# Kernel tuning notes

Measured on AMD Instinct MI355X. Metric: run time of the kernel, lower is better.

Reference implementation:

```python
import jax, jax.numpy as jnp
import numpy as np

N = 4096        # nodes
E = 131072      # edges (avg degree 32)
D = 128         # parser.d
H1, H2, H3 = 256, 128, 64   # parser.neurons_gnn
L = 2
THRESH = 0.6 ** L           # cosine-similarity cutoff used in attention()
SCALE = 0.05                # weight init scale


def setup_inputs() -> dict:
    key = jax.random.key(0)
    ks = jax.random.split(key, 14)
    X = jax.random.normal(ks[0], (N, D), dtype=jnp.float32)
    edge_index = jax.random.randint(ks[1], (2, E), 0, N, dtype=jnp.int64)
    W1 = jax.random.normal(ks[2], (D, H1), dtype=jnp.float32) * SCALE
    b1 = jnp.zeros((H1,), dtype=jnp.float32)
    a1w = jax.random.normal(ks[3], (2 * H1,), dtype=jnp.float32) * SCALE
    a1b = jnp.zeros((), dtype=jnp.float32)
    W2 = jax.random.normal(ks[4], (H1, H2), dtype=jnp.float32) * SCALE
    b2 = jnp.zeros((H2,), dtype=jnp.float32)
    a2w = jax.random.normal(ks[5], (2 * H2,), dtype=jnp.float32) * SCALE
    a2b = jnp.zeros((), dtype=jnp.float32)
    W3 = jax.random.normal(ks[6], (H2, H3), dtype=jnp.float32) * SCALE
    b3 = jnp.zeros((H3,), dtype=jnp.float32)
    return {"X": X, "edge_index": edge_index,
            "W1": W1, "b1": b1, "a1w": a1w, "a1b": a1b,
            "W2": W2, "b2": b2, "a2w": a2w, "a2b": a2b,
            "W3": W3, "b3": b3}


def _attention(h, src, dst, aw, ab):
    """Vectorized form of GNN.attention: edge-softmax neighbor aggregation
    plus dense cosine-thresholded all-pairs aggregation, averaged.
    attn_fc(cat(h_i, h_j)) = (h_i . aw_left) + (h_j . aw_right) + ab."""
    n, dh = h.shape
    al = h @ aw[:dh]            # [N] left half of attention projection
    ar = h @ aw[dh:]            # [N] right half
    # --- neighbor branch: a_ij = softmax-like normalized exp(leaky_relu(.)) over neighbors of i
    e = jnp.exp(jax.nn.leaky_relu(al[src] + ar[dst] + ab))   # [E]
    denom = jax.ops.segment_sum(e, src, num_segments=n)      # [N]
    a = e / denom[src]                                       # [E]
    h_a = h + jax.ops.segment_sum(a[:, None] * h[dst], src, num_segments=n)
    # --- dense branch: thresholded cosine similarity modulates attention score
    hn = h / jnp.linalg.norm(h, axis=1, keepdims=True)       # [N, dh]
    C = hn @ hn.T                                            # [N, N] cosine
    C = jnp.where(C <= THRESH, 0.0, C)
    S = al[:, None] + ar[None, :] + ab                       # [N, N] attn scores
    B = jnp.exp(C * jax.nn.leaky_relu(S))                    # [N, N]
    h1 = h + B @ h
    return 0.5 * (h_a + h1)


def reference(X, edge_index, W1, b1, a1w, a1b, W2, b2, a2w, a2b, W3, b3):
    src, dst = edge_index[0], edge_index[1]
    h = X @ W1 + b1
    h = _attention(h, src, dst, a1w, a1b)
    h = jax.nn.relu(h)
    h = h @ W2 + b2
    h = _attention(h, src, dst, a2w, a2b)
    h = jax.nn.relu(h)
    h = h @ W3 + b3
    # F.normalize(h, p=2, dim=1)
    h = h / jnp.maximum(jnp.linalg.norm(h, axis=1, keepdims=True), 1e-12)
    return h
```

## Files before the change

kernel.cpp:

```cpp
#include <hip/hip_runtime.h>
#include <math.h>
#include <type_traits>

#define NN 4096
#define NE 131072

typedef short short8 __attribute__((ext_vector_type(8)));
typedef float f32x4 __attribute__((ext_vector_type(4)));
typedef float f32x2 __attribute__((ext_vector_type(2)));
typedef unsigned short u16;

__device__ __forceinline__ float lrelu_f(float x) { return x > 0.0f ? x : 0.01f * x; }

__device__ __forceinline__ u16 f2bf(float x) {
  unsigned int u = __float_as_uint(x);
  unsigned int r = (u + 0x7FFF + ((u >> 16) & 1)) >> 16;
  return (u16)r;
}
__device__ __forceinline__ float bf2f(u16 b) { return __uint_as_float(((unsigned int)b) << 16); }

__device__ __forceinline__ void gload_lds16(const u16* g, u16* l) {
  __builtin_amdgcn_global_load_lds((const __attribute__((address_space(1))) void*)g,
                                   (__attribute__((address_space(3))) void*)l, 16, 0, 0);
}

__global__ __launch_bounds__(256) void wtrans_kernel(const float* __restrict__ W,
    u16* __restrict__ WThi, u16* __restrict__ WTlo, int K, int P) {
  __shared__ u16 th[32][33], tl[32][33];
  int bp = blockIdx.x, bk = blockIdx.y;
  int t = threadIdx.x, tx = t & 31, ty8 = t >> 5;
  #pragma unroll
  for (int r = 0; r < 4; ++r) {
    int k = bk * 32 + ty8 + r * 8;
    int p = bp * 32 + tx;
    float x = W[(size_t)k * P + p];
    u16 hi = f2bf(x);
    th[ty8 + r * 8][tx] = hi;
    tl[ty8 + r * 8][tx] = f2bf(x - bf2f(hi));
  }
  __syncthreads();
  #pragma unroll
  for (int r = 0; r < 4; ++r) {
    int p = bp * 32 + ty8 + r * 8;
    int k = bk * 32 + tx;
    WThi[(size_t)p * K + k] = th[tx][ty8 + r * 8];
    WTlo[(size_t)p * K + k] = tl[tx][ty8 + r * 8];
  }
}

template<bool RELU>
__global__ __launch_bounds__(256) void convert_io_kernel(const float* __restrict__ x,
    u16* __restrict__ ghi, u16* __restrict__ glo) {
  int idx = blockIdx.x * 256 + threadIdx.x;
  float v = x[idx];
  if (RELU) v = fmaxf(v, 0.0f);
  u16 hi = f2bf(v);
  ghi[idx] = hi;
  glo[idx] = f2bf(v - bf2f(hi));
}

template<int K, int P>
__global__ __launch_bounds__(256) void mgemm_kernel(
    const u16* __restrict__ Ahi, const u16* __restrict__ Alo,
    const u16* __restrict__ WThi, const u16* __restrict__ WTlo,
    const float* __restrict__ bias, float* __restrict__ O) {
  constexpr int KC = K / 32;
  int w = threadIdx.x >> 6, l = threadIdx.x & 63;
  int lr = l & 15, lk = l >> 4;
  int i0 = blockIdx.x * 16;
  int p0 = blockIdx.y * 64 + w * 16;
  const u16* arh = Ahi + (size_t)(i0 + lr) * K + lk * 8;
  const u16* arl = Alo + (size_t)(i0 + lr) * K + lk * 8;
  const u16* brh = WThi + (size_t)(p0 + lr) * K + lk * 8;
  const u16* brl = WTlo + (size_t)(p0 + lr) * K + lk * 8;
  f32x4 ahh = {0.f, 0.f, 0.f, 0.f};
  f32x4 ahl = {0.f, 0.f, 0.f, 0.f};
  f32x4 alh = {0.f, 0.f, 0.f, 0.f};
  #pragma unroll
  for (int c = 0; c < KC; ++c) {
    short8 Ah = *(const short8*)(arh + 32 * c);
    short8 Al = *(const short8*)(arl + 32 * c);
    short8 Bh = *(const short8*)(brh + 32 * c);
    short8 Bl = *(const short8*)(brl + 32 * c);
    ahh = __builtin_amdgcn_mfma_f32_16x16x32_bf16(Ah, Bh, ahh, 0, 0, 0);
    ahl = __builtin_amdgcn_mfma_f32_16x16x32_bf16(Ah, Bl, ahl, 0, 0, 0);
    alh = __builtin_amdgcn_mfma_f32_16x16x32_bf16(Al, Bh, alh, 0, 0, 0);
  }
  int p = p0 + lr;
  float bv = bias[p];
  #pragma unroll
  for (int q = 0; q < 4; ++q) {
    int i = i0 + 4 * lk + q;
    O[(size_t)i * P + p] = ahh[q] + ahl[q] + alh[q] + bv;
  }
}

template<int DH>
__global__ __launch_bounds__(256) void rowstats_kernel(const float* __restrict__ h,
    const float* __restrict__ aw, float* __restrict__ al, float* __restrict__ ar,
    float* __restrict__ inv) {
  constexpr int NC = DH / 64;
  int wid = threadIdx.x >> 6, lane = threadIdx.x & 63;
  int i = blockIdx.x * 4 + wid;
  float s2 = 0.f, sl = 0.f, sr = 0.f;
  #pragma unroll
  for (int c = 0; c < NC; ++c) {
    float x = h[(size_t)i * DH + c * 64 + lane];
    s2 = fmaf(x, x, s2);
    sl = fmaf(x, aw[c * 64 + lane], sl);
    sr = fmaf(x, aw[DH + c * 64 + lane], sr);
  }
  #pragma unroll
  for (int m = 32; m > 0; m >>= 1) {
    s2 += __shfl_xor(s2, m);
    sl += __shfl_xor(sl, m);
    sr += __shfl_xor(sr, m);
  }
  if (lane == 0) { al[i] = sl; ar[i] = sr; inv[i] = rsqrtf(s2); }
}

template<int DH>
__global__ void colsum_kernel(const float* __restrict__ h, float* __restrict__ cs) {
  int d = threadIdx.x;
  int r0 = blockIdx.x * (NN / 32);
  float s = 0.f;
  for (int i = 0; i < NN / 32; ++i) s += h[(size_t)(r0 + i) * DH + d];
  atomicAdd(&cs[d], s);
}

template<int DH>
__global__ __launch_bounds__(256) void convtrans_kernel(const float* __restrict__ h,
    u16* __restrict__ hhi, u16* __restrict__ hlo, u16* __restrict__ hT) {
  __shared__ u16 tile[32][33];
  int bx = blockIdx.x;
  int by = blockIdx.y;
  int t = threadIdx.x, tx = t & 31, ty8 = t >> 5;
  #pragma unroll
  for (int r = 0; r < 4; ++r) {
    int i = by * 32 + ty8 + r * 8;
    int d = bx * 32 + tx;
    float x = h[(size_t)i * DH + d];
    u16 hi = f2bf(x);
    hhi[(size_t)i * DH + d] = hi;
    hlo[(size_t)i * DH + d] = f2bf(x - bf2f(hi));
    tile[ty8 + r * 8][tx] = hi;
  }
  __syncthreads();
  #pragma unroll
  for (int r = 0; r < 4; ++r) {
    int d = bx * 32 + ty8 + r * 8;
    int i = by * 32 + tx;
    hT[(size_t)d * NN + i] = tile[tx][ty8 + r * 8];
  }
}

__global__ void hist_kernel(const int* __restrict__ src, int* __restrict__ counts) {
  int e = blockIdx.x * 256 + threadIdx.x;
  atomicAdd(&counts[src[e]], 1);
}

__global__ __launch_bounds__(1024) void scan_kernel(const int* __restrict__ counts,
    int* __restrict__ offsets, int* __restrict__ cursor) {
  __shared__ int part[1024];
  int t = threadIdx.x;
  int v[4]; int run = 0;
  #pragma unroll
  for (int j = 0; j < 4; ++j) { v[j] = counts[4 * t + j]; run += v[j]; }
  part[t] = run;
  __syncthreads();
  for (int off = 1; off < 1024; off <<= 1) {
    int y = (t >= off) ? part[t - off] : 0;
    __syncthreads();
    part[t] += y;
    __syncthreads();
  }
  int base = part[t] - run;
  #pragma unroll
  for (int j = 0; j < 4; ++j) { offsets[4 * t + j] = base; cursor[4 * t + j] = base; base += v[j]; }
  if (t == 1023) offsets[NN] = base;
}

__global__ void scatter_idx_kernel(const int* __restrict__ src, const int* __restrict__ dst,
    int* __restrict__ cursor, int* __restrict__ dstS) {
  int e = blockIdx.x * 256 + threadIdx.x;
  int s = src[e];
  int p = atomicAdd(&cursor[s], 1);
  dstS[p] = dst[e];
}

template<int DH>
__global__ __launch_bounds__(256) void gather_kernel(const float* __restrict__ h,
    const int* __restrict__ offsets, const int* __restrict__ dstS,
    const float* __restrict__ al, const float* __restrict__ ar,
    const float* __restrict__ ab, float* __restrict__ o) {
  constexpr int VW = DH / 64;
  using V = typename std::conditional<VW == 4, f32x4, f32x2>::type;
  int wid = threadIdx.x >> 6, lane = threadIdx.x & 63;
  int i = blockIdx.x * 4 + wid;
  int beg = offsets[i], end = offsets[i + 1];
  float base = al[i] + ab[0];
  V acc0{}, acc1{};
  float esum0 = 0.f, esum1 = 0.f;
  int k = beg;
  for (; k + 2 <= end; k += 2) {
    int d0 = dstS[k], d1 = dstS[k + 1];
    float e0 = expf(lrelu_f(base + ar[d0]));
    float e1 = expf(lrelu_f(base + ar[d1]));
    V v0 = *(const V*)&h[(size_t)d0 * DH + lane * VW];
    V v1 = *(const V*)&h[(size_t)d1 * DH + lane * VW];
    esum0 += e0; esum1 += e1;
    acc0 += e0 * v0;
    acc1 += e1 * v1;
  }
  if (k < end) {
    int d0 = dstS[k];
    float e0 = expf(lrelu_f(base + ar[d0]));
    V v0 = *(const V*)&h[(size_t)d0 * DH + lane * VW];
    esum0 += e0;
    acc0 += e0 * v0;
  }
  float esum = esum0 + esum1;
  float rd = (beg < end) ? 0.5f / esum : 0.0f;
  *(V*)&o[(size_t)i * DH + lane * VW] = (acc0 + acc1) * rd;
}

template<int DH>
__global__ __launch_bounds__(256) void qk_kernel(
    const u16* __restrict__ hhi, const u16* __restrict__ hlo,
    const float* __restrict__ al, const float* __restrict__ ar,
    const float* __restrict__ inv, const float* __restrict__ ab,
    u16* __restrict__ W, int* __restrict__ flags) {
  constexpr int KC = DH / 32;
  __shared__ u16 sA[2][2][128][32];
  __shared__ u16 sB[2][2][128][32];
  int i0 = blockIdx.x * 128;
  int j0 = blockIdx.y * 128;
  int w = threadIdx.x >> 6, l = threadIdx.x & 63;
  int wr = w >> 1, wc = w & 1;
  int lr = l & 15, lk = l >> 4;

  int rl = l >> 2;
  int sc = ((l & 3) ^ ((l >> 3) & 3)) * 8;
  const u16* gAh0 = hhi + (size_t)(i0 + 32 * w + rl) * DH + sc;
  const u16* gAl0 = hlo + (size_t)(i0 + 32 * w + rl) * DH + sc;
  const u16* gBh0 = hhi + (size_t)(j0 + 32 * w + rl) * DH + sc;
  const u16* gBl0 = hlo + (size_t)(j0 + 32 * w + rl) * DH + sc;

  f32x4 acc[4][4];
  #pragma unroll
  for (int q = 0; q < 4; ++q)
    #pragma unroll
    for (int s = 0; s < 4; ++s) acc[q][s] = (f32x4){0.f, 0.f, 0.f, 0.f};

#define QK_STAGE(buf, c) do { \
    gload_lds16(gAh0 + (c) * 32,           &sA[buf][0][32 * w][0]); \
    gload_lds16(gAh0 + 16 * DH + (c) * 32, &sA[buf][0][32 * w + 16][0]); \
    gload_lds16(gAl0 + (c) * 32,           &sA[buf][1][32 * w][0]); \
    gload_lds16(gAl0 + 16 * DH + (c) * 32, &sA[buf][1][32 * w + 16][0]); \
    gload_lds16(gBh0 + (c) * 32,           &sB[buf][0][32 * w][0]); \
    gload_lds16(gBh0 + 16 * DH + (c) * 32, &sB[buf][0][32 * w + 16][0]); \
    gload_lds16(gBl0 + (c) * 32,           &sB[buf][1][32 * w][0]); \
    gload_lds16(gBl0 + 16 * DH + (c) * 32, &sB[buf][1][32 * w + 16][0]); \
  } while (0)

  QK_STAGE(0, 0);
  __syncthreads();

  int cs = (lk ^ ((lr >> 1) & 3)) * 8;
  int cur = 0;
  for (int c = 0; c < KC; ++c) {
    if (c + 1 < KC) QK_STAGE(cur ^ 1, c + 1);
    short8 Ah[4], Al[4], Bh[4], Bl[4];
    #pragma unroll
    for (int q = 0; q < 4; ++q) {
      Ah[q] = *(const short8*)&sA[cur][0][64 * wr + 16 * q + lr][cs];
      Al[q] = *(const short8*)&sA[cur][1][64 * wr + 16 * q + lr][cs];
    }
    #pragma unroll
    for (int s = 0; s < 4; ++s) {
      Bh[s] = *(const short8*)&sB[cur][0][64 * wc + 16 * s + lr][cs];
      Bl[s] = *(const short8*)&sB[cur][1][64 * wc + 16 * s + lr][cs];
    }
    #pragma unroll
    for (int q = 0; q < 4; ++q)
      #pragma unroll
      for (int s = 0; s < 4; ++s) {
        acc[q][s] = __builtin_amdgcn_mfma_f32_16x16x32_bf16(Al[q], Bh[s], acc[q][s], 0, 0, 0);
        acc[q][s] = __builtin_amdgcn_mfma_f32_16x16x32_bf16(Ah[q], Bl[s], acc[q][s], 0, 0, 0);
        acc[q][s] = __builtin_amdgcn_mfma_f32_16x16x32_bf16(Ah[q], Bh[s], acc[q][s], 0, 0, 0);
      }
    __syncthreads();
    cur ^= 1;
  }
#undef QK_STAGE

  float abv = ab[0];
  int i_base = i0 + 64 * wr + 4 * lk;
  int j_base = j0 + 64 * wc + lr;
  float arj[4], invj[4];
  #pragma unroll
  for (int s = 0; s < 4; ++s) {
    int j = j_base + 16 * s;
    arj[s] = ar[j] + abv;
    invj[s] = inv[j];
  }
  int wany = 0;
  #pragma unroll
  for (int q = 0; q < 4; ++q) {
    float ali_[4], invi_[4];
    #pragma unroll
    for (int qq = 0; qq < 4; ++qq) {
      int i = i_base + 16 * q + qq;
      ali_[qq] = al[i];
      invi_[qq] = inv[i];
    }
    #pragma unroll
    for (int s = 0; s < 4; ++s)
      #pragma unroll
      for (int qq = 0; qq < 4; ++qq) {
        float C = acc[q][s][qq] * invi_[qq] * invj[s];
        float wv = 0.0f;
        if (C > 0.36f) wv = expm1f(C * lrelu_f(ali_[qq] + arj[s]));
        if (wv != 0.0f) wany = 1;
        W[(size_t)(i_base + 16 * q + qq) * NN + j_base + 16 * s] = f2bf(wv);
      }
  }
  int anyv = __any(wany) ? 1 : 0;
  if (l == 0)
    flags[((i0 >> 6) + wr) * 64 + (j0 >> 6) + wc] = anyv;
}

template<int DH>
__global__ __launch_bounds__(256) void pv_kernel(
    const u16* __restrict__ W, const u16* __restrict__ hT,
    const int* __restrict__ flags, const float* __restrict__ h,
    const float* __restrict__ cs, float* __restrict__ o) {
  __shared__ u16 sW[2][16][64];
  __shared__ u16 sT[2][4][16][64];
  __shared__ int list[64];
  __shared__ int nact_s;
  int ib = blockIdx.x;
  int w = threadIdx.x >> 6, l = threadIdx.x & 63;
  int lr = l & 15, lk = l >> 4;
  int i0 = ib * 16;
  int d0 = blockIdx.y * 64 + w * 16;
  const int* frow = flags + (i0 >> 6) * 64;
  if (threadIdx.x < 64) {
    int f = frow[threadIdx.x] != 0;
    unsigned long long m = __ballot(f);
    int pos = __popcll(m & ((1ULL << threadIdx.x) - 1ULL));
    if (f) list[pos] = threadIdx.x;
    if (threadIdx.x == 0) nact_s = __popcll(m);
  }
  __syncthreads();
  int nact = nact_s;

  int srow0 = l >> 3;
  int scol = ((l & 7) * 8) ^ ((srow0 & 7) << 3);
  const u16* gW0 = W + (size_t)(i0 + srow0) * NN + scol;
  const u16* gT0 = hT + (size_t)(d0 + srow0) * NN + scol;
  f32x4 acc0 = {0.f, 0.f, 0.f, 0.f};
  f32x4 acc1 = {0.f, 0.f, 0.f, 0.f};

  if (nact > 0) {
    {
      int j0 = list[0] * 64;
      if (w == 0) {
        gload_lds16(gW0 + j0, &sW[0][0][0]);
        gload_lds16(gW0 + 8 * NN + j0, &sW[0][8][0]);
      }
      gload_lds16(gT0 + j0, &sT[0][w][0][0]);
      gload_lds16(gT0 + 8 * NN + j0, &sT[0][w][8][0]);
    }
    __syncthreads();
    int cur = 0;
    for (int t = 0; t < nact; ++t) {
      if (t + 1 < nact) {
        int jn = list[t + 1] * 64;
        int nb = cur ^ 1;
        if (w == 0) {
          gload_lds16(gW0 + jn, &sW[nb][0][0]);
          gload_lds16(gW0 + 8 * NN + jn, &sW[nb][8][0]);
        }
        gload_lds16(gT0 + jn, &sT[nb][w][0][0]);
        gload_lds16(gT0 + 8 * NN + jn, &sT[nb][w][8][0]);
      }
      int sx = (lr & 7) << 3;
      short8 a0 = *(const short8*)&sW[cur][lr][(lk * 8) ^ sx];
      short8 a1 = *(const short8*)&sW[cur][lr][(32 + lk * 8) ^ sx];
      short8 b0 = *(const short8*)&sT[cur][w][lr][(lk * 8) ^ sx];
      short8 b1 = *(const short8*)&sT[cur][w][lr][(32 + lk * 8) ^ sx];
      acc0 = __builtin_amdgcn_mfma_f32_16x16x32_bf16(a0, b0, acc0, 0, 0, 0);
      acc1 = __builtin_amdgcn_mfma_f32_16x16x32_bf16(a1, b1, acc1, 0, 0, 0);
      __syncthreads();
      cur ^= 1;
    }
  }

  int d = d0 + lr;
  #pragma unroll
  for (int q = 0; q < 4; ++q) {
    int i = i0 + 4 * lk + q;
    size_t idx = (size_t)i * DH + d;
    o[idx] = o[idx] + h[idx] + 0.5f * cs[d] + 0.5f * (acc0[q] + acc1[q]);
  }
}

__global__ __launch_bounds__(256) void norm_kernel(float* __restrict__ out) {
  int wid = threadIdx.x >> 6, lane = threadIdx.x & 63;
  int i = blockIdx.x * 4 + wid;
  float x = out[(size_t)i * 64 + lane];
  float s = x * x;
  #pragma unroll
  for (int m = 32; m > 0; m >>= 1) s += __shfl_xor(s, m);
  float n = sqrtf(s);
  out[(size_t)i * 64 + lane] = x / fmaxf(n, 1e-12f);
}

struct Scratch {
  float *al, *ar, *inv, *cs;
  int *counts, *offsets, *cursor, *dstS, *flags;
  u16 *hhi, *hlo, *hT, *W;
  u16 *ghi, *glo, *wthi, *wtlo;
};

template<int DH>
static void run_attention(const float* h, const float* aw, const float* ab, float* o,
                          const Scratch& S, hipStream_t stream) {
  rowstats_kernel<DH><<<NN / 4, 256, 0, stream>>>(h, aw, S.al, S.ar, S.inv);
  hipMemsetAsync(S.cs, 0, DH * sizeof(float), stream);
  colsum_kernel<DH><<<32, DH, 0, stream>>>(h, S.cs);
  convtrans_kernel<DH><<<dim3(DH / 32, NN / 32), 256, 0, stream>>>(h, S.hhi, S.hlo, S.hT);
  gather_kernel<DH><<<NN / 4, 256, 0, stream>>>(h, S.offsets, S.dstS, S.al, S.ar, ab, o);
  qk_kernel<DH><<<dim3(NN / 128, NN / 128), 256, 0, stream>>>(
      S.hhi, S.hlo, S.al, S.ar, S.inv, ab, S.W, S.flags);
  pv_kernel<DH><<<dim3(NN / 16, DH / 64), 256, 0, stream>>>(
      S.W, S.hT, S.flags, h, S.cs, o);
}

extern "C" void kernel_launch(void* const* d_in, const int* in_sizes, int n_in,
                              void* d_out, int out_size, void* d_ws, size_t ws_size,
                              hipStream_t stream) {
  const float* X   = (const float*)d_in[0];
  const int*   ei  = (const int*)d_in[1];
  const float* W1  = (const float*)d_in[2];
  const float* b1  = (const float*)d_in[3];
  const float* a1w = (const float*)d_in[4];
  const float* a1b = (const float*)d_in[5];
  const float* W2  = (const float*)d_in[6];
  const float* b2  = (const float*)d_in[7];
  const float* a2w = (const float*)d_in[8];
  const float* a2b = (const float*)d_in[9];
  const float* W3  = (const float*)d_in[10];
  const float* b3  = (const float*)d_in[11];
  float* out = (float*)d_out;

  const int* src = ei;
  const int* dst = ei + NE;

  char* p = (char*)d_ws;
  auto alloc = [&](size_t bytes) { char* r = p; p += (bytes + 255) & ~(size_t)255; return r; };
  float* h1 = (float*)alloc((size_t)NN * 256 * 4);
  float* o1 = (float*)alloc((size_t)NN * 256 * 4);
  float* h2 = (float*)alloc((size_t)NN * 128 * 4);
  float* o2 = (float*)alloc((size_t)NN * 128 * 4);
  Scratch S;
  S.hhi = (u16*)alloc((size_t)NN * 256 * 2);
  S.hlo = (u16*)alloc((size_t)NN * 256 * 2);
  S.hT  = (u16*)alloc((size_t)NN * 256 * 2);
  S.W   = (u16*)alloc((size_t)NN * NN * 2);
  S.ghi = (u16*)alloc((size_t)NN * 256 * 2);
  S.glo = (u16*)alloc((size_t)NN * 256 * 2);
  S.wthi = (u16*)alloc((size_t)256 * 256 * 2);
  S.wtlo = (u16*)alloc((size_t)256 * 256 * 2);
  S.flags = (int*)alloc(4096 * 4);
  S.al    = (float*)alloc(NN * 4);
  S.ar    = (float*)alloc(NN * 4);
  S.inv   = (float*)alloc(NN * 4);
  S.cs    = (float*)alloc(256 * 4);
  S.counts  = (int*)alloc(NN * 4);
  S.offsets = (int*)alloc((NN + 1) * 4);
  S.cursor  = (int*)alloc(NN * 4);
  S.dstS    = (int*)alloc((size_t)NE * 4);

  hipMemsetAsync(S.counts, 0, NN * sizeof(int), stream);
  hist_kernel<<<NE / 256, 256, 0, stream>>>(src, S.counts);
  scan_kernel<<<1, 1024, 0, stream>>>(S.counts, S.offsets, S.cursor);
  scatter_idx_kernel<<<NE / 256, 256, 0, stream>>>(src, dst, S.cursor, S.dstS);

  wtrans_kernel<<<dim3(256 / 32, 128 / 32), 256, 0, stream>>>(W1, S.wthi, S.wtlo, 128, 256);
  convert_io_kernel<false><<<NN * 128 / 256, 256, 0, stream>>>(X, S.ghi, S.glo);
  mgemm_kernel<128, 256><<<dim3(NN / 16, 256 / 64), 256, 0, stream>>>(
      S.ghi, S.glo, S.wthi, S.wtlo, b1, h1);
  run_attention<256>(h1, a1w, a1b, o1, S, stream);

  wtrans_kernel<<<dim3(128 / 32, 256 / 32), 256, 0, stream>>>(W2, S.wthi, S.wtlo, 256, 128);
  convert_io_kernel<true><<<NN * 256 / 256, 256, 0, stream>>>(o1, S.ghi, S.glo);
  mgemm_kernel<256, 128><<<dim3(NN / 16, 128 / 64), 256, 0, stream>>>(
      S.ghi, S.glo, S.wthi, S.wtlo, b2, h2);
  run_attention<128>(h2, a2w, a2b, o2, S, stream);

  wtrans_kernel<<<dim3(64 / 32, 128 / 32), 256, 0, stream>>>(W3, S.wthi, S.wtlo, 128, 64);
  convert_io_kernel<true><<<NN * 128 / 256, 256, 0, stream>>>(o2, S.ghi, S.glo);
  mgemm_kernel<128, 64><<<dim3(NN / 16, 64 / 64), 256, 0, stream>>>(
      S.ghi, S.glo, S.wthi, S.wtlo, b3, out);
  norm_kernel<<<NN / 4, 256, 0, stream>>>(out);
}
```

Before: 265.5 us.

## Fuse small prep kernels: weight transposes, input conversion, row stats, final normalize

Three weight-transpose launches are merged into one kernel, and the fp32-to-split-bf16 input conversion (with ReLU) moves inside the GEMM kernel. The final L2 normalize is folded into the last GEMM's epilogue. Row stats, column sums, bf16 conversion and transpose become a single prep kernel per attention layer, and the memsets are combined into one. This removes many small launches and intermediate global round trips. In exchange the GEMM redoes the conversion per column block, and the transpose is now written with 16-row tiles.

```diff
diff --git a/kernel.cpp b/kernel.cpp
--- a/kernel.cpp
+++ b/kernel.cpp
@@ -24,10 +24,17 @@
                                    (__attribute__((address_space(3))) void*)l, 16, 0, 0);
 }
 
-__global__ __launch_bounds__(256) void wtrans_kernel(const float* __restrict__ W,
-    u16* __restrict__ WThi, u16* __restrict__ WTlo, int K, int P) {
+__global__ __launch_bounds__(256) void wtrans_all_kernel(
+    const float* __restrict__ W1, const float* __restrict__ W2, const float* __restrict__ W3,
+    u16* __restrict__ w1h, u16* __restrict__ w1l,
+    u16* __restrict__ w2h, u16* __restrict__ w2l,
+    u16* __restrict__ w3h, u16* __restrict__ w3l) {
   __shared__ u16 th[32][33], tl[32][33];
-  int bp = blockIdx.x, bk = blockIdx.y;
+  const float* W; u16 *oh, *ol; int K, P, bp, bk;
+  int bx = blockIdx.x;
+  if (bx < 32)      { W = W1; oh = w1h; ol = w1l; K = 128; P = 256; int b = bx;      bp = b & 7; bk = b >> 3; }
+  else if (bx < 64) { W = W2; oh = w2h; ol = w2l; K = 256; P = 128; int b = bx - 32; bp = b & 3; bk = b >> 2; }
+  else              { W = W3; oh = w3h; ol = w3l; K = 128; P = 64;  int b = bx - 64; bp = b & 1; bk = b >> 1; }
   int t = threadIdx.x, tx = t & 31, ty8 = t >> 5;
   #pragma unroll
   for (int r = 0; r < 4; ++r) {
@@ -43,34 +50,23 @@
   for (int r = 0; r < 4; ++r) {
     int p = bp * 32 + ty8 + r * 8;
     int k = bk * 32 + tx;
-    WThi[(size_t)p * K + k] = th[tx][ty8 + r * 8];
-    WTlo[(size_t)p * K + k] = tl[tx][ty8 + r * 8];
-  }
-}
-
-template<bool RELU>
-__global__ __launch_bounds__(256) void convert_io_kernel(const float* __restrict__ x,
-    u16* __restrict__ ghi, u16* __restrict__ glo) {
-  int idx = blockIdx.x * 256 + threadIdx.x;
-  float v = x[idx];
-  if (RELU) v = fmaxf(v, 0.0f);
-  u16 hi = f2bf(v);
-  ghi[idx] = hi;
-  glo[idx] = f2bf(v - bf2f(hi));
-}
-
-template<int K, int P>
+    oh[(size_t)p * K + k] = th[tx][ty8 + r * 8];
+    ol[(size_t)p * K + k] = tl[tx][ty8 + r * 8];
+  }
+}
+
+template<int K, int P, bool RELU, bool NORM>
 __global__ __launch_bounds__(256) void mgemm_kernel(
-    const u16* __restrict__ Ahi, const u16* __restrict__ Alo,
+    const float* __restrict__ A,
     const u16* __restrict__ WThi, const u16* __restrict__ WTlo,
     const float* __restrict__ bias, float* __restrict__ O) {
   constexpr int KC = K / 32;
+  __shared__ float ldsn[4][16];
   int w = threadIdx.x >> 6, l = threadIdx.x & 63;
   int lr = l & 15, lk = l >> 4;
   int i0 = blockIdx.x * 16;
   int p0 = blockIdx.y * 64 + w * 16;
-  const u16* arh = Ahi + (size_t)(i0 + lr) * K + lk * 8;
-  const u16* arl = Alo + (size_t)(i0 + lr) * K + lk * 8;
+  const float* ar_ = A + (size_t)(i0 + lr) * K + lk * 8;
   const u16* brh = WThi + (size_t)(p0 + lr) * K + lk * 8;
   const u16* brl = WTlo + (size_t)(p0 + lr) * K + lk * 8;
   f32x4 ahh = {0.f, 0.f, 0.f, 0.f};
@@ -78,8 +74,18 @@
   f32x4 alh = {0.f, 0.f, 0.f, 0.f};
   #pragma unroll
   for (int c = 0; c < KC; ++c) {
-    short8 Ah = *(const short8*)(arh + 32 * c);
-    short8 Al = *(const short8*)(arl + 32 * c);
+    f32x4 a0 = *(const f32x4*)(ar_ + 32 * c);
+    f32x4 a1 = *(const f32x4*)(ar_ + 32 * c + 4);
+    float av[8] = {a0[0], a0[1], a0[2], a0[3], a1[0], a1[1], a1[2], a1[3]};
+    short8 Ah, Al;
+    #pragma unroll
+    for (int j = 0; j < 8; ++j) {
+      float x = av[j];
+      if (RELU) x = fmaxf(x, 0.0f);
+      u16 hi = f2bf(x);
+      Ah[j] = (short)hi;
+      Al[j] = (short)f2bf(x - bf2f(hi));
+    }
     short8 Bh = *(const short8*)(brh + 32 * c);
     short8 Bl = *(const short8*)(brl + 32 * c);
     ahh = __builtin_amdgcn_mfma_f32_16x16x32_bf16(Ah, Bh, ahh, 0, 0, 0);
@@ -88,69 +94,119 @@
   }
   int p = p0 + lr;
   float bv = bias[p];
-  #pragma unroll
-  for (int q = 0; q < 4; ++q) {
-    int i = i0 + 4 * lk + q;
-    O[(size_t)i * P + p] = ahh[q] + ahl[q] + alh[q] + bv;
+  float ov[4];
+  #pragma unroll
+  for (int q = 0; q < 4; ++q) ov[q] = ahh[q] + ahl[q] + alh[q] + bv;
+
+  if (NORM) {
+    float sq[4];
+    #pragma unroll
+    for (int q = 0; q < 4; ++q) {
+      float s = ov[q] * ov[q];
+      #pragma unroll
+      for (int m = 1; m < 16; m <<= 1) s += __shfl_xor(s, m);
+      sq[q] = s;
+    }
+    if (lr == 0) {
+      #pragma unroll
+      for (int q = 0; q < 4; ++q) ldsn[w][4 * lk + q] = sq[q];
+    }
+    __syncthreads();
+    #pragma unroll
+    for (int q = 0; q < 4; ++q) {
+      int row = 4 * lk + q;
+      float n2 = ldsn[0][row] + ldsn[1][row] + ldsn[2][row] + ldsn[3][row];
+      float nf = 1.0f / fmaxf(sqrtf(n2), 1e-12f);
+      int i = i0 + row;
+      O[(size_t)i * P + p] = ov[q] * nf;
+    }
+  } else {
+    #pragma unroll
+    for (int q = 0; q < 4; ++q) {
+      int i = i0 + 4 * lk + q;
+      O[(size_t)i * P + p] = ov[q];
+    }
   }
 }
 
 template<int DH>
-__global__ __launch_bounds__(256) void rowstats_kernel(const float* __restrict__ h,
+__global__ __launch_bounds__(256) void prep_kernel(const float* __restrict__ h,
     const float* __restrict__ aw, float* __restrict__ al, float* __restrict__ ar,
-    float* __restrict__ inv) {
-  constexpr int NC = DH / 64;
-  int wid = threadIdx.x >> 6, lane = threadIdx.x & 63;
-  int i = blockIdx.x * 4 + wid;
+    float* __restrict__ inv, float* __restrict__ cs,
+    u16* __restrict__ hhi, u16* __restrict__ hlo, u16* __restrict__ hT) {
+  constexpr int CPT = DH / 16;
+  __shared__ u16 tile[16][DH + 8];
+  __shared__ float ldsp[4][DH];
+  int t = threadIdx.x;
+  int w = t >> 6, l = t & 63;
+  int rw = l >> 4;
+  int row = w * 4 + rw;
+  int tcol = l & 15;
+  int i = blockIdx.x * 16 + row;
+  int c0 = tcol * CPT;
+
+  float v[CPT];
+  const float* hr = h + (size_t)i * DH + c0;
+  #pragma unroll
+  for (int k = 0; k < CPT; k += 4) {
+    f32x4 x = *(const f32x4*)(hr + k);
+    v[k] = x[0]; v[k + 1] = x[1]; v[k + 2] = x[2]; v[k + 3] = x[3];
+  }
   float s2 = 0.f, sl = 0.f, sr = 0.f;
   #pragma unroll
-  for (int c = 0; c < NC; ++c) {
-    float x = h[(size_t)i * DH + c * 64 + lane];
-    s2 = fmaf(x, x, s2);
-    sl = fmaf(x, aw[c * 64 + lane], sl);
-    sr = fmaf(x, aw[DH + c * 64 + lane], sr);
-  }
-  #pragma unroll
-  for (int m = 32; m > 0; m >>= 1) {
+  for (int k = 0; k < CPT; ++k) {
+    s2 = fmaf(v[k], v[k], s2);
+    sl = fmaf(v[k], aw[c0 + k], sl);
+    sr = fmaf(v[k], aw[DH + c0 + k], sr);
+  }
+  #pragma unroll
+  for (int m = 1; m < 16; m <<= 1) {
     s2 += __shfl_xor(s2, m);
     sl += __shfl_xor(sl, m);
     sr += __shfl_xor(sr, m);
   }
-  if (lane == 0) { al[i] = sl; ar[i] = sr; inv[i] = rsqrtf(s2); }
-}
-
-template<int DH>
-__global__ void colsum_kernel(const float* __restrict__ h, float* __restrict__ cs) {
-  int d = threadIdx.x;
-  int r0 = blockIdx.x * (NN / 32);
-  float s = 0.f;
-  for (int i = 0; i < NN / 32; ++i) s += h[(size_t)(r0 + i) * DH + d];
-  atomicAdd(&cs[d], s);
-}
-
-template<int DH>
-__global__ __launch_bounds__(256) void convtrans_kernel(const float* __restrict__ h,
-    u16* __restrict__ hhi, u16* __restrict__ hlo, u16* __restrict__ hT) {
-  __shared__ u16 tile[32][33];
-  int bx = blockIdx.x;
-  int by = blockIdx.y;
-  int t = threadIdx.x, tx = t & 31, ty8 = t >> 5;
-  #pragma unroll
-  for (int r = 0; r < 4; ++r) {
-    int i = by * 32 + ty8 + r * 8;
-    int d = bx * 32 + tx;
-    float x = h[(size_t)i * DH + d];
+  if (tcol == 0) { al[i] = sl; ar[i] = sr; inv[i] = rsqrtf(s2); }
+
+  u16 hiv[CPT];
+  short8 hs[CPT / 8], ls[CPT / 8];
+  #pragma unroll
+  for (int k = 0; k < CPT; ++k) {
+    float x = v[k];
     u16 hi = f2bf(x);
-    hhi[(size_t)i * DH + d] = hi;
-    hlo[(size_t)i * DH + d] = f2bf(x - bf2f(hi));
-    tile[ty8 + r * 8][tx] = hi;
+    hiv[k] = hi;
+    hs[k / 8][k & 7] = (short)hi;
+    ls[k / 8][k & 7] = (short)f2bf(x - bf2f(hi));
+  }
+  #pragma unroll
+  for (int b = 0; b < CPT / 8; ++b) {
+    *(short8*)&hhi[(size_t)i * DH + c0 + b * 8] = hs[b];
+    *(short8*)&hlo[(size_t)i * DH + c0 + b * 8] = ls[b];
+    *(short8*)&tile[row][c0 + b * 8] = hs[b];
+  }
+  float colp[CPT];
+  #pragma unroll
+  for (int k = 0; k < CPT; ++k) {
+    float s = v[k];
+    s += __shfl_xor(s, 16);
+    s += __shfl_xor(s, 32);
+    colp[k] = s;
+  }
+  if (rw == 0) {
+    #pragma unroll
+    for (int k = 0; k < CPT; ++k) ldsp[w][c0 + k] = colp[k];
   }
   __syncthreads();
-  #pragma unroll
-  for (int r = 0; r < 4; ++r) {
-    int d = bx * 32 + ty8 + r * 8;
-    int i = by * 32 + tx;
-    hT[(size_t)d * NN + i] = tile[tx][ty8 + r * 8];
+  if (t < DH) {
+    float s = ldsp[0][t] + ldsp[1][t] + ldsp[2][t] + ldsp[3][t];
+    atomicAdd(&cs[t], s);
+    int i0 = blockIdx.x * 16;
+    short8 o0, o1;
+    #pragma unroll
+    for (int r = 0; r < 8; ++r) o0[r] = (short)tile[r][t];
+    #pragma unroll
+    for (int r = 0; r < 8; ++r) o1[r] = (short)tile[8 + r][t];
+    *(short8*)&hT[(size_t)t * NN + i0] = o0;
+    *(short8*)&hT[(size_t)t * NN + i0 + 8] = o1;
   }
 }
 
@@ -406,36 +462,23 @@
   }
 }
 
-__global__ __launch_bounds__(256) void norm_kernel(float* __restrict__ out) {
-  int wid = threadIdx.x >> 6, lane = threadIdx.x & 63;
-  int i = blockIdx.x * 4 + wid;
-  float x = out[(size_t)i * 64 + lane];
-  float s = x * x;
-  #pragma unroll
-  for (int m = 32; m > 0; m >>= 1) s += __shfl_xor(s, m);
-  float n = sqrtf(s);
-  out[(size_t)i * 64 + lane] = x / fmaxf(n, 1e-12f);
-}
-
 struct Scratch {
-  float *al, *ar, *inv, *cs;
+  float *al, *ar, *inv, *cs1, *cs2;
   int *counts, *offsets, *cursor, *dstS, *flags;
   u16 *hhi, *hlo, *hT, *W;
-  u16 *ghi, *glo, *wthi, *wtlo;
+  u16 *w1h, *w1l, *w2h, *w2l, *w3h, *w3l;
 };
 
 template<int DH>
 static void run_attention(const float* h, const float* aw, const float* ab, float* o,
-                          const Scratch& S, hipStream_t stream) {
-  rowstats_kernel<DH><<<NN / 4, 256, 0, stream>>>(h, aw, S.al, S.ar, S.inv);
-  hipMemsetAsync(S.cs, 0, DH * sizeof(float), stream);
-  colsum_kernel<DH><<<32, DH, 0, stream>>>(h, S.cs);
-  convtrans_kernel<DH><<<dim3(DH / 32, NN / 32), 256, 0, stream>>>(h, S.hhi, S.hlo, S.hT);
+                          float* cs, const Scratch& S, hipStream_t stream) {
+  prep_kernel<DH><<<NN / 16, 256, 0, stream>>>(h, aw, S.al, S.ar, S.inv, cs,
+                                               S.hhi, S.hlo, S.hT);
   gather_kernel<DH><<<NN / 4, 256, 0, stream>>>(h, S.offsets, S.dstS, S.al, S.ar, ab, o);
   qk_kernel<DH><<<dim3(NN / 128, NN / 128), 256, 0, stream>>>(
       S.hhi, S.hlo, S.al, S.ar, S.inv, ab, S.W, S.flags);
   pv_kernel<DH><<<dim3(NN / 16, DH / 64), 256, 0, stream>>>(
-      S.W, S.hT, S.flags, h, S.cs, o);
+      S.W, S.hT, S.flags, h, cs, o);
 }
 
 extern "C" void kernel_launch(void* const* d_in, const int* in_sizes, int n_in,
@@ -465,44 +508,42 @@
   float* h2 = (float*)alloc((size_t)NN * 128 * 4);
   float* o2 = (float*)alloc((size_t)NN * 128 * 4);
   Scratch S;
+  S.counts = (int*)alloc(NN * 4);
+  S.cs1    = (float*)alloc(256 * 4);
+  S.cs2    = (float*)alloc(128 * 4);
   S.hhi = (u16*)alloc((size_t)NN * 256 * 2);
   S.hlo = (u16*)alloc((size_t)NN * 256 * 2);
   S.hT  = (u16*)alloc((size_t)NN * 256 * 2);
   S.W   = (u16*)alloc((size_t)NN * NN * 2);
-  S.ghi = (u16*)alloc((size_t)NN * 256 * 2);
-  S.glo = (u16*)alloc((size_t)NN * 256 * 2);
-  S.wthi = (u16*)alloc((size_t)256 * 256 * 2);
-  S.wtlo = (u16*)alloc((size_t)256 * 256 * 2);
+  S.w1h = (u16*)alloc((size_t)256 * 128 * 2);
+  S.w1l = (u16*)alloc((size_t)256 * 128 * 2);
+  S.w2h = (u16*)alloc((size_t)128 * 256 * 2);
+  S.w2l = (u16*)alloc((size_t)128 * 256 * 2);
+  S.w3h = (u16*)alloc((size_t)64 * 128 * 2);
+  S.w3l = (u16*)alloc((size_t)64 * 128 * 2);
   S.flags = (int*)alloc(4096 * 4);
   S.al    = (float*)alloc(NN * 4);
   S.ar    = (float*)alloc(NN * 4);
   S.inv   = (float*)alloc(NN * 4);
-  S.cs    = (float*)alloc(256 * 4);
-  S.counts  = (int*)alloc(NN * 4);
   S.offsets = (int*)alloc((NN + 1) * 4);
   S.cursor  = (int*)alloc(NN * 4);
   S.dstS    = (int*)alloc((size_t)NE * 4);
 
-  hipMemsetAsync(S.counts, 0, NN * sizeof(int), stream);
+  hipMemsetAsync(S.counts, 0, NN * 4 + 256 * 4 + 128 * 4, stream);
   hist_kernel<<<NE / 256, 256, 0, stream>>>(src, S.counts);
   scan_kernel<<<1, 1024, 0, stream>>>(S.counts, S.offsets, S.cursor);
   scatter_idx_kernel<<<NE / 256, 256, 0, stream>>>(src, dst, S.cursor, S.dstS);
-
-  wtrans_kernel<<<dim3(256 / 32, 128 / 32), 256, 0, stream>>>(W1, S.wthi, S.wtlo, 128, 256);
-  convert_io_kernel<false><<<NN * 128 / 256, 256, 0, stream>>>(X, S.ghi, S.glo);
-  mgemm_kernel<128, 256><<<dim3(NN / 16, 256 / 64), 256, 0, stream>>>(
-      S.ghi, S.glo, S.wthi, S.wtlo, b1, h1);
-  run_attention<256>(h1, a1w, a1b, o1, S, stream);
-
-  wtrans_kernel<<<dim3(128 / 32, 256 / 32), 256, 0, stream>>>(W2, S.wthi, S.wtlo, 256, 128);
-  convert_io_kernel<true><<<NN * 256 / 256, 256, 0, stream>>>(o1, S.ghi, S.glo);
-  mgemm_kernel<256, 128><<<dim3(NN / 16, 128 / 64), 256, 0, stream>>>(
-      S.ghi, S.glo, S.wthi, S.wtlo, b2, h2);
-  run_attention<128>(h2, a2w, a2b, o2, S, stream);
-
-  wtrans_kernel<<<dim3(64 / 32, 128 / 32), 256, 0, stream>>>(W3, S.wthi, S.wtlo, 128, 64);
-  convert_io_kernel<true><<<NN * 128 / 256, 256, 0, stream>>>(o2, S.ghi, S.glo);
-  mgemm_kernel<128, 64><<<dim3(NN / 16, 64 / 64), 256, 0, stream>>>(
-      S.ghi, S.glo, S.wthi, S.wtlo, b3, out);
-  norm_kernel<<<NN / 4, 256, 0, stream>>>(out);
-}
+  wtrans_all_kernel<<<72, 256, 0, stream>>>(W1, W2, W3,
+      S.w1h, S.w1l, S.w2h, S.w2l, S.w3h, S.w3l);
+
+  mgemm_kernel<128, 256, false, false><<<dim3(NN / 16, 256 / 64), 256, 0, stream>>>(
+      X, S.w1h, S.w1l, b1, h1);
+  run_attention<256>(h1, a1w, a1b, o1, S.cs1, S, stream);
+
+  mgemm_kernel<256, 128, true, false><<<dim3(NN / 16, 128 / 64), 256, 0, stream>>>(
+      o1, S.w2h, S.w2l, b2, h2);
+  run_attention<128>(h2, a2w, a2b, o2, S.cs2, S, stream);
+
+  mgemm_kernel<128, 64, true, true><<<dim3(NN / 16, 64 / 64), 256, 0, stream>>>(
+      o2, S.w3h, S.w3l, b3, out);
+}
```

Result: faster. 250.1 us (-5.8%).
